# Kernel tuning notes

Measured on AMD Instinct MI355X. Metric: run time of the kernel, lower is better.

## Reference

```python
import jax, jax.numpy as jnp
import numpy as np

HID = 512
HEADS = 8
HEAD_DIM = HID // HEADS
B, S = 2, 4096


def setup_inputs() -> dict:
    key = jax.random.key(0)
    ks = jax.random.split(key, 11)
    sc = 0.02
    return {
        "query": jax.random.normal(ks[0], (B, S, HID), jnp.float32),
        "key": jax.random.normal(ks[1], (B, S, HID), jnp.float32),
        "value": jax.random.normal(ks[2], (B, S, HID), jnp.float32),
        "Wq": jax.random.normal(ks[3], (HID, HID), jnp.float32) * sc,
        "bq": jax.random.normal(ks[4], (HID,), jnp.float32) * sc,
        "Wk": jax.random.normal(ks[5], (HID, HID), jnp.float32) * sc,
        "bk": jax.random.normal(ks[6], (HID,), jnp.float32) * sc,
        "Wv": jax.random.normal(ks[7], (HID, HID), jnp.float32) * sc,
        "bv": jax.random.normal(ks[8], (HID,), jnp.float32) * sc,
        "Wo": jax.random.normal(ks[9], (HID, HID), jnp.float32) * sc,
        "bo": jax.random.normal(ks[10], (HID,), jnp.float32) * sc,
    }


def reference(query, key, value, Wq, bq, Wk, bk, Wv, bv, Wo, bo):
    b, s, _ = query.shape
    scale = jnp.sqrt(jnp.float32(HEAD_DIM))
    # projections (nn.Linear: x @ W.T + b)
    Q = query @ Wq.T + bq
    K = key @ Wk.T + bk
    V = value @ Wv.T + bv
    # split heads: [b, h, s, d]
    Q = Q.reshape(b, s, HEADS, HEAD_DIM).transpose(0, 2, 1, 3)
    K = K.reshape(b, s, HEADS, HEAD_DIM).transpose(0, 2, 1, 3)
    V = V.reshape(b, s, HEADS, HEAD_DIM).transpose(0, 2, 1, 3)
    # scaled dot-product attention (mask=None, dropout in eval mode = identity)
    energy = jnp.einsum('bhqd,bhkd->bhqk', Q, K) / scale
    attention = jax.nn.softmax(energy, axis=-1)
    x = jnp.einsum('bhqk,bhkd->bhqd', attention, V)
    x = x.transpose(0, 2, 1, 3).reshape(b, s, HID)
    return x @ Wo.T + bo
```

## Files before the change

kernel.cpp:

```cpp
#include <hip/hip_runtime.h>
#include <stdint.h>

#define HID 512
#define NH 8
#define HD 64
#define BATCH 2
#define SEQ 4096
#define M_TOT (BATCH*SEQ)
#define NBH (BATCH*NH)
#define SPLITK 4

typedef __attribute__((ext_vector_type(8))) short short8;
typedef __attribute__((ext_vector_type(4))) short short4v;
typedef __attribute__((ext_vector_type(4))) float floatx4;
typedef unsigned short u16;

__device__ inline u16 f2bf(float x) {
  unsigned u = __builtin_bit_cast(unsigned, x);
  unsigned r = u + 0x7fff + ((u >> 16) & 1);
  return (u16)(r >> 16);
}

__device__ inline float bf2f(u16 h) {
  unsigned u = ((unsigned)h) << 16;
  return __builtin_bit_cast(float, u);
}

__device__ inline unsigned pack_bf16(float a, float b) {
  unsigned ua = __builtin_bit_cast(unsigned, a) + 0x8000u;
  unsigned ub = __builtin_bit_cast(unsigned, b) + 0x8000u;
  return __builtin_amdgcn_perm(ub, ua, 0x07060302u);
}

__device__ inline void gll16(const void* g, void* l) {
  __builtin_amdgcn_global_load_lds((const __attribute__((address_space(1))) void*)g,
                                   (__attribute__((address_space(3))) void*)l, 16, 0, 0);
}


__global__ void cvt_all(const float* __restrict__ q, const float* __restrict__ k,
                        const float* __restrict__ v, const float* __restrict__ wq,
                        const float* __restrict__ wk, const float* __restrict__ wv,
                        const float* __restrict__ wo,
                        u16* __restrict__ xq, u16* __restrict__ xk,
                        u16* __restrict__ xv, u16* __restrict__ wb) {
  const size_t NW = (size_t)HID * HID;
  int bx = (int)blockIdx.x;
  const float* src; u16* dst; int blk;
  if (bx < 12288) {
    int seg = bx >> 12;
    blk = bx & 4095;
    src = (seg == 0) ? q : ((seg == 1) ? k : v);
    dst = (seg == 0) ? xq : ((seg == 1) ? xk : xv);
  } else {
    int w = (bx - 12288) >> 8;
    blk = (bx - 12288) & 255;
    src = (w == 0) ? wq : ((w == 1) ? wk : ((w == 2) ? wv : wo));
    dst = wb + (size_t)w * NW;
  }
  int i = (blk * 256 + (int)threadIdx.x) * 4;
  const float4 val = *(const float4*)(src + i);
  union { uint2 u; u16 h[4]; } pk;
  pk.h[0] = f2bf(val.x); pk.h[1] = f2bf(val.y);
  pk.h[2] = f2bf(val.z); pk.h[3] = f2bf(val.w);
  *(uint2*)(dst + i) = pk.u;
}

__global__ __launch_bounds__(256) void gemm_qkv(
    const u16* __restrict__ Xq, const u16* __restrict__ Xk, const u16* __restrict__ Xv,
    const u16* __restrict__ Wb,
    const float* __restrict__ bq, const float* __restrict__ bk, const float* __restrict__ bv,
    u16* __restrict__ Qp, u16* __restrict__ Kp, u16* __restrict__ Vt) {
  const int z = blockIdx.z;
  const u16* X = (z == 0) ? Xq : ((z == 1) ? Xk : Xv);
  const u16* W = Wb + (size_t)z * (HID * HID);
  const float* bias = (z == 0) ? bq : ((z == 1) ? bk : bv);

  __shared__ u16 As[128 * 32];
  __shared__ u16 Bs[128 * 32];

  const int tid = threadIdx.x;
  const int wid = tid >> 6, lane = tid & 63;
  const int wm = wid >> 1, wn = wid & 1;
  const int quad = lane >> 4, l16 = lane & 15;
  const int m0 = (int)blockIdx.x * 128, n0 = (int)blockIdx.y * 128;
  const int srow = lane >> 2;
  const int scol = (lane & 3) * 8;

  floatx4 acc[4][4];
#pragma unroll
  for (int i = 0; i < 4; i++)
#pragma unroll
    for (int j = 0; j < 4; j++) acc[i][j] = floatx4{0.f, 0.f, 0.f, 0.f};

  for (int k0 = 0; k0 < HID; k0 += 32) {
#pragma unroll
    for (int r = 0; r < 2; r++) {
      int row = r * 64 + wid * 16 + srow;
      gll16(X + (size_t)(m0 + row) * HID + k0 + scol, &As[(r * 64 + wid * 16) * 32]);
      gll16(W + (size_t)(n0 + row) * HID + k0 + scol, &Bs[(r * 64 + wid * 16) * 32]);
    }
    __syncthreads();
    short8 af[4], bf[4];
#pragma unroll
    for (int mt = 0; mt < 4; mt++)
      af[mt] = *(const short8*)&As[(wm * 64 + mt * 16 + l16) * 32 + quad * 8];
#pragma unroll
    for (int nt = 0; nt < 4; nt++)
      bf[nt] = *(const short8*)&Bs[(wn * 64 + nt * 16 + l16) * 32 + quad * 8];
#pragma unroll
    for (int mt = 0; mt < 4; mt++)
#pragma unroll
      for (int nt = 0; nt < 4; nt++)
        acc[mt][nt] = __builtin_amdgcn_mfma_f32_16x16x32_bf16(af[mt], bf[nt], acc[mt][nt], 0, 0, 0);
    __syncthreads();
  }

#pragma unroll
  for (int mt = 0; mt < 4; mt++) {
#pragma unroll
    for (int nt = 0; nt < 4; nt++) {
      int ncol = n0 + wn * 64 + nt * 16 + l16;
      float bias_v = bias[ncol];
      int h = ncol >> 6, d = ncol & 63;
#pragma unroll
      for (int r = 0; r < 4; r++) {
        int mrow = m0 + wm * 64 + mt * 16 + quad * 4 + r;
        float v = acc[mt][nt][r] + bias_v;
        int b = mrow >> 12, s = mrow & (SEQ - 1);
        size_t base = (size_t)(b * NH + h) * SEQ * HD;
        if (z == 2) {
          size_t idx = base + (size_t)(s >> 4) * 1024 + (d >> 4) * 256 + ((s >> 2) & 3) * 64 + (d & 15) * 4 + (s & 3);
          Vt[idx] = f2bf(v);
        } else {
          size_t idx = base + (size_t)(s >> 4) * 1024 + (d >> 3) * 128 + (s & 15) * 8 + (d & 7);
          if (z == 0) Qp[idx] = f2bf(v * 0.18033688f);
          else        Kp[idx] = f2bf(v);
        }
      }
    }
  }
}

__global__ __launch_bounds__(256) void gemm_out(
    const u16* __restrict__ X, const u16* __restrict__ W,
    const float* __restrict__ bias, float* __restrict__ out) {
  __shared__ u16 As[128 * 32];
  __shared__ u16 Bs[64 * 32];

  const int tid = threadIdx.x;
  const int wid = tid >> 6, lane = tid & 63;
  const int wm = wid >> 1, wn = wid & 1;
  const int quad = lane >> 4, l16 = lane & 15;
  const int m0 = (int)blockIdx.x * 128, n0 = (int)blockIdx.y * 64;
  const int srow = lane >> 2;
  const int scol = (lane & 3) * 8;

  floatx4 acc[4][2];
#pragma unroll
  for (int i = 0; i < 4; i++)
#pragma unroll
    for (int j = 0; j < 2; j++) acc[i][j] = floatx4{0.f, 0.f, 0.f, 0.f};

  for (int k0 = 0; k0 < HID; k0 += 32) {
#pragma unroll
    for (int r = 0; r < 2; r++) {
      int row = r * 64 + wid * 16 + srow;
      gll16(X + (size_t)(m0 + row) * HID + k0 + scol, &As[(r * 64 + wid * 16) * 32]);
    }
    {
      int row = wid * 16 + srow;
      gll16(W + (size_t)(n0 + row) * HID + k0 + scol, &Bs[(wid * 16) * 32]);
    }
    __syncthreads();
    short8 af[4], bf[2];
#pragma unroll
    for (int mt = 0; mt < 4; mt++)
      af[mt] = *(const short8*)&As[(wm * 64 + mt * 16 + l16) * 32 + quad * 8];
#pragma unroll
    for (int nt = 0; nt < 2; nt++)
      bf[nt] = *(const short8*)&Bs[(wn * 32 + nt * 16 + l16) * 32 + quad * 8];
#pragma unroll
    for (int mt = 0; mt < 4; mt++)
#pragma unroll
      for (int nt = 0; nt < 2; nt++)
        acc[mt][nt] = __builtin_amdgcn_mfma_f32_16x16x32_bf16(af[mt], bf[nt], acc[mt][nt], 0, 0, 0);
    __syncthreads();
  }

#pragma unroll
  for (int mt = 0; mt < 4; mt++) {
#pragma unroll
    for (int nt = 0; nt < 2; nt++) {
      int ncol = n0 + wn * 32 + nt * 16 + l16;
      float bias_v = bias[ncol];
#pragma unroll
      for (int r = 0; r < 4; r++) {
        int mrow = m0 + wm * 64 + mt * 16 + quad * 4 + r;
        out[(size_t)mrow * HID + ncol] = acc[mt][nt][r] + bias_v;
      }
    }
  }
}

__global__ __launch_bounds__(256) void attn_kernel(
    const u16* __restrict__ Qp, const u16* __restrict__ Kp,
    const u16* __restrict__ Vt, u16* __restrict__ Opb, float* __restrict__ Lp) {
  const int bh = blockIdx.y;
  const int sp = blockIdx.z;
  const int q0 = (int)blockIdx.x * 128;
  const u16* Qh = Qp + (size_t)bh * SEQ * HD;
  const u16* Kh = Kp + (size_t)bh * SEQ * HD;
  const u16* Vh = Vt + (size_t)bh * SEQ * HD;

  __shared__ u16 Ks[2][4096];
  __shared__ u16 Vs[2][4096];

  const int tid = threadIdx.x;
  const int wid = tid >> 6, lane = tid & 63;
  const int quad = lane >> 4, l16 = lane & 15;

  short8 qf[2][2];
#pragma unroll
  for (int kq = 0; kq < 2; kq++)
#pragma unroll
    for (int n = 0; n < 2; n++)
      qf[kq][n] = *(const short8*)(Qh + (size_t)(q0 / 16 + wid * 2 + n) * 1024 + (kq * 4 + quad) * 128 + l16 * 8);

  float l_part[2] = {0.f, 0.f};
  floatx4 o[2][4];
#pragma unroll
  for (int m = 0; m < 2; m++)
#pragma unroll
    for (int dt = 0; dt < 4; dt++) o[m][dt] = floatx4{0.f, 0.f, 0.f, 0.f};

  const int kv_lo = sp * (SEQ / SPLITK), kv_hi = kv_lo + SEQ / SPLITK;

  auto stage = [&](int buf, int kv0) {
    const u16* kg = Kh + (size_t)(kv0 >> 4) * 1024;
    const u16* vg = Vh + (size_t)(kv0 >> 4) * 1024;
#pragma unroll
    for (int r = 0; r < 2; r++) {
      int c = wid + r * 4;
      gll16(kg + c * 512 + lane * 8, &Ks[buf][c * 512]);
      gll16(vg + c * 512 + lane * 8, &Vs[buf][c * 512]);
    }
  };

  stage(0, kv_lo);
  __syncthreads();

  int ibuf = 0;
  for (int kv0 = kv_lo; kv0 < kv_hi; kv0 += 64) {
    if (kv0 + 64 < kv_hi) stage(ibuf ^ 1, kv0 + 64);

#pragma unroll
    for (int t = 0; t < 4; t++) {
      short8 ak0 = *(const short8*)&Ks[ibuf][t * 1024 + (0 * 4 + quad) * 128 + l16 * 8];
      short8 ak1 = *(const short8*)&Ks[ibuf][t * 1024 + (1 * 4 + quad) * 128 + l16 * 8];
      short4v vf[4];
#pragma unroll
      for (int dt = 0; dt < 4; dt++)
        vf[dt] = *(const short4v*)&Vs[ibuf][t * 1024 + dt * 256 + quad * 64 + l16 * 4];

      floatx4 st[2];
      st[0] = __builtin_amdgcn_mfma_f32_16x16x32_bf16(ak0, qf[0][0], floatx4{0.f,0.f,0.f,0.f}, 0, 0, 0);
      st[1] = __builtin_amdgcn_mfma_f32_16x16x32_bf16(ak0, qf[0][1], floatx4{0.f,0.f,0.f,0.f}, 0, 0, 0);
      st[0] = __builtin_amdgcn_mfma_f32_16x16x32_bf16(ak1, qf[1][0], st[0], 0, 0, 0);
      st[1] = __builtin_amdgcn_mfma_f32_16x16x32_bf16(ak1, qf[1][1], st[1], 0, 0, 0);

#pragma unroll
      for (int n = 0; n < 2; n++) {
        float p0 = __builtin_amdgcn_exp2f(st[n][0]);
        float p1 = __builtin_amdgcn_exp2f(st[n][1]);
        float p2 = __builtin_amdgcn_exp2f(st[n][2]);
        float p3 = __builtin_amdgcn_exp2f(st[n][3]);
        l_part[n] += (p0 + p1) + (p2 + p3);
        union { unsigned u[2]; short4v s; } pk;
        pk.u[0] = pack_bf16(p0, p1);
        pk.u[1] = pack_bf16(p2, p3);
#pragma unroll
        for (int dt = 0; dt < 4; dt++)
          o[n][dt] = __builtin_amdgcn_mfma_f32_16x16x16bf16_1k(pk.s, vf[dt], o[n][dt], 0, 0, 0);
      }
    }
    __syncthreads();
    ibuf ^= 1;
  }

#pragma unroll
  for (int n = 0; n < 2; n++) {
    l_part[n] += __shfl_xor(l_part[n], 16);
    l_part[n] += __shfl_xor(l_part[n], 32);
  }
  u16* Oph = Opb + (size_t)(sp * NBH + bh) * SEQ * HD;
  float* Lph = Lp + (size_t)(sp * NBH + bh) * SEQ;
  if (quad == 0) {
#pragma unroll
    for (int n = 0; n < 2; n++)
      Lph[q0 + wid * 32 + n * 16 + l16] = l_part[n];
  }
#pragma unroll
  for (int m = 0; m < 2; m++) {
#pragma unroll
    for (int r = 0; r < 4; r++) {
      int s = q0 + wid * 32 + m * 16 + quad * 4 + r;
#pragma unroll
      for (int dt = 0; dt < 4; dt++)
        Oph[(size_t)s * HD + dt * 16 + l16] = f2bf(o[m][dt][r]);
    }
  }
}

__global__ __launch_bounds__(256) void combine_kernel(
    const u16* __restrict__ Opb, const float* __restrict__ Lp, u16* __restrict__ Xo) {
  int idx = (int)blockIdx.x * 256 + (int)threadIdx.x;
  int e = idx * 4;
  int bh = e >> 18;
  int rem = e & 262143;
  int q = rem >> 6, d = rem & 63;
  float acc0 = 0.f, acc1 = 0.f, acc2 = 0.f, acc3 = 0.f, lsum = 0.f;
#pragma unroll
  for (int sp = 0; sp < SPLITK; sp++) {
    size_t i = ((size_t)(sp * NBH + bh) * SEQ + q) * HD + d;
    union { uint2 u; u16 h[4]; } pk;
    pk.u = *(const uint2*)(Opb + i);
    acc0 += bf2f(pk.h[0]); acc1 += bf2f(pk.h[1]);
    acc2 += bf2f(pk.h[2]); acc3 += bf2f(pk.h[3]);
    lsum += Lp[(size_t)(sp * NBH + bh) * SEQ + q];
  }
  float inv = 1.f / lsum;
  int b = bh >> 3, h = bh & 7;
  u16* dst = Xo + ((size_t)(b * SEQ + q)) * HID + h * HD + d;
  union { uint2 u; u16 hh[4]; } pk;
  pk.hh[0] = f2bf(acc0 * inv);
  pk.hh[1] = f2bf(acc1 * inv);
  pk.hh[2] = f2bf(acc2 * inv);
  pk.hh[3] = f2bf(acc3 * inv);
  *(uint2*)dst = pk.u;
}

extern "C" void kernel_launch(void* const* d_in, const int* in_sizes, int n_in,
                              void* d_out, int out_size, void* d_ws, size_t ws_size,
                              hipStream_t stream) {
  const float* q  = (const float*)d_in[0];
  const float* k  = (const float*)d_in[1];
  const float* v  = (const float*)d_in[2];
  const float* Wq = (const float*)d_in[3];
  const float* bq = (const float*)d_in[4];
  const float* Wk = (const float*)d_in[5];
  const float* bk = (const float*)d_in[6];
  const float* Wv = (const float*)d_in[7];
  const float* bv = (const float*)d_in[8];
  const float* Wo = (const float*)d_in[9];
  const float* bo = (const float*)d_in[10];

  u16* wsb = (u16*)d_ws;
  const size_t NW = (size_t)HID * HID;
  const size_t NX = (size_t)M_TOT * HID;
  u16* Wb = wsb;
  u16* Xq = wsb + 4 * NW;
  u16* Xk = Xq + NX;
  u16* Xv = Xk + NX;
  u16* Qp = Xv + NX;
  u16* Kp = Qp + NX;
  u16* Vt = Kp + NX;
  u16* Xo = Vt + NX;
  u16* Opb = Xo + NX;
  float* Lp = (float*)(Opb + (size_t)SPLITK * NBH * SEQ * HD);

  dim3 blk(256);
  cvt_all<<<dim3(13312), blk, 0, stream>>>(q, k, v, Wq, Wk, Wv, Wo, Xq, Xk, Xv, Wb);

  gemm_qkv<<<dim3(64, 4, 3), blk, 0, stream>>>(Xq, Xk, Xv, Wb, bq, bk, bv, Qp, Kp, Vt);
  attn_kernel<<<dim3(32, NBH, SPLITK), blk, 0, stream>>>(Qp, Kp, Vt, Opb, Lp);
  combine_kernel<<<dim3(4096), blk, 0, stream>>>(Opb, Lp, Xo);
  gemm_out<<<dim3(64, 8), blk, 0, stream>>>(Xo, Wb + 3 * NW, bo, (float*)d_out);
}
```

Measured before the change: 236.3 us.

## Use 16x16x32 MFMA for PV product with 32-key V layout and hardware bf16 pack

Changes the V tensor layout so 32 consecutive keys per d-column are contiguous. This lets the attention kernel process two 16-key score tiles at once and run the P·V product with the 16x16x32 bf16 MFMA instead of 16x16x16. It halves the number of PV MFMA issues and replaces the manual round-and-perm bf16 packing with the v_cvt_pk_bf16_f32 instruction. Costs are more live registers per iteration and a rounding mode that may differ slightly from the previous manual rounding.

Result: faster. 230.7 us (-2.3%).

```diff
diff --git a/kernel.cpp b/kernel.cpp
--- a/kernel.cpp
+++ b/kernel.cpp
@@ -11,7 +11,6 @@
 #define SPLITK 4
 
 typedef __attribute__((ext_vector_type(8))) short short8;
-typedef __attribute__((ext_vector_type(4))) short short4v;
 typedef __attribute__((ext_vector_type(4))) float floatx4;
 typedef unsigned short u16;
 
@@ -26,10 +25,10 @@
   return __builtin_bit_cast(float, u);
 }
 
-__device__ inline unsigned pack_bf16(float a, float b) {
-  unsigned ua = __builtin_bit_cast(unsigned, a) + 0x8000u;
-  unsigned ub = __builtin_bit_cast(unsigned, b) + 0x8000u;
-  return __builtin_amdgcn_perm(ub, ua, 0x07060302u);
+__device__ inline unsigned cvt_pk_bf16(float a, float b) {
+  unsigned r;
+  asm("v_cvt_pk_bf16_f32 %0, %1, %2" : "=v"(r) : "v"(a), "v"(b));
+  return r;
 }
 
 __device__ inline void gll16(const void* g, void* l) {
@@ -130,7 +129,8 @@
         int b = mrow >> 12, s = mrow & (SEQ - 1);
         size_t base = (size_t)(b * NH + h) * SEQ * HD;
         if (z == 2) {
-          size_t idx = base + (size_t)(s >> 4) * 1024 + (d >> 4) * 256 + ((s >> 2) & 3) * 64 + (d & 15) * 4 + (s & 3);
+          size_t idx = base + (size_t)(s >> 5) * 2048 + (d >> 4) * 512 + (d & 15) * 32
+                     + ((s >> 2) & 3) * 8 + ((s >> 4) & 1) * 4 + (s & 3);
           Vt[idx] = f2bf(v);
         } else {
           size_t idx = base + (size_t)(s >> 4) * 1024 + (d >> 3) * 128 + (s & 15) * 8 + (d & 7);
@@ -255,33 +255,45 @@
     if (kv0 + 64 < kv_hi) stage(ibuf ^ 1, kv0 + 64);
 
 #pragma unroll
-    for (int t = 0; t < 4; t++) {
-      short8 ak0 = *(const short8*)&Ks[ibuf][t * 1024 + (0 * 4 + quad) * 128 + l16 * 8];
-      short8 ak1 = *(const short8*)&Ks[ibuf][t * 1024 + (1 * 4 + quad) * 128 + l16 * 8];
-      short4v vf[4];
+    for (int gg = 0; gg < 2; gg++) {
+      const u16* Kb = &Ks[ibuf][gg * 2048];
+      short8 akA0 = *(const short8*)&Kb[quad * 128 + l16 * 8];
+      short8 akA1 = *(const short8*)&Kb[(4 + quad) * 128 + l16 * 8];
+      short8 akB0 = *(const short8*)&Kb[1024 + quad * 128 + l16 * 8];
+      short8 akB1 = *(const short8*)&Kb[1024 + (4 + quad) * 128 + l16 * 8];
+      short8 vf[4];
 #pragma unroll
       for (int dt = 0; dt < 4; dt++)
-        vf[dt] = *(const short4v*)&Vs[ibuf][t * 1024 + dt * 256 + quad * 64 + l16 * 4];
-
-      floatx4 st[2];
-      st[0] = __builtin_amdgcn_mfma_f32_16x16x32_bf16(ak0, qf[0][0], floatx4{0.f,0.f,0.f,0.f}, 0, 0, 0);
-      st[1] = __builtin_amdgcn_mfma_f32_16x16x32_bf16(ak0, qf[0][1], floatx4{0.f,0.f,0.f,0.f}, 0, 0, 0);
-      st[0] = __builtin_amdgcn_mfma_f32_16x16x32_bf16(ak1, qf[1][0], st[0], 0, 0, 0);
-      st[1] = __builtin_amdgcn_mfma_f32_16x16x32_bf16(ak1, qf[1][1], st[1], 0, 0, 0);
-
+        vf[dt] = *(const short8*)&Vs[ibuf][gg * 2048 + dt * 512 + l16 * 32 + quad * 8];
+
+      floatx4 stA[2], stB[2];
 #pragma unroll
       for (int n = 0; n < 2; n++) {
-        float p0 = __builtin_amdgcn_exp2f(st[n][0]);
-        float p1 = __builtin_amdgcn_exp2f(st[n][1]);
-        float p2 = __builtin_amdgcn_exp2f(st[n][2]);
-        float p3 = __builtin_amdgcn_exp2f(st[n][3]);
-        l_part[n] += (p0 + p1) + (p2 + p3);
-        union { unsigned u[2]; short4v s; } pk;
-        pk.u[0] = pack_bf16(p0, p1);
-        pk.u[1] = pack_bf16(p2, p3);
+        stA[n] = __builtin_amdgcn_mfma_f32_16x16x32_bf16(akA0, qf[0][n], floatx4{0.f,0.f,0.f,0.f}, 0, 0, 0);
+        stB[n] = __builtin_amdgcn_mfma_f32_16x16x32_bf16(akB0, qf[0][n], floatx4{0.f,0.f,0.f,0.f}, 0, 0, 0);
+        stA[n] = __builtin_amdgcn_mfma_f32_16x16x32_bf16(akA1, qf[1][n], stA[n], 0, 0, 0);
+        stB[n] = __builtin_amdgcn_mfma_f32_16x16x32_bf16(akB1, qf[1][n], stB[n], 0, 0, 0);
+      }
+
+#pragma unroll
+      for (int n = 0; n < 2; n++) {
+        float a0 = __builtin_amdgcn_exp2f(stA[n][0]);
+        float a1 = __builtin_amdgcn_exp2f(stA[n][1]);
+        float a2 = __builtin_amdgcn_exp2f(stA[n][2]);
+        float a3 = __builtin_amdgcn_exp2f(stA[n][3]);
+        float b0 = __builtin_amdgcn_exp2f(stB[n][0]);
+        float b1 = __builtin_amdgcn_exp2f(stB[n][1]);
+        float b2 = __builtin_amdgcn_exp2f(stB[n][2]);
+        float b3 = __builtin_amdgcn_exp2f(stB[n][3]);
+        l_part[n] += ((a0 + a1) + (a2 + a3)) + ((b0 + b1) + (b2 + b3));
+        union { unsigned u[4]; short8 s; } pk;
+        pk.u[0] = cvt_pk_bf16(a0, a1);
+        pk.u[1] = cvt_pk_bf16(a2, a3);
+        pk.u[2] = cvt_pk_bf16(b0, b1);
+        pk.u[3] = cvt_pk_bf16(b2, b3);
 #pragma unroll
         for (int dt = 0; dt < 4; dt++)
-          o[n][dt] = __builtin_amdgcn_mfma_f32_16x16x16bf16_1k(pk.s, vf[dt], o[n][dt], 0, 0, 0);
+          o[n][dt] = __builtin_amdgcn_mfma_f32_16x16x32_bf16(pk.s, vf[dt], o[n][dt], 0, 0, 0);
       }
     }
     __syncthreads();
```
